# Optimization experiments

Measured on AMD Instinct MI355X. Metric: run time of the kernel, lower is better.

The kernel has to match this reference:

```python
import jax, jax.numpy as jnp
import numpy as np

B, T, D = 8, 1024, 768
H, HD = 12, 64
DFF = 3072
EPS = 1e-5


def setup_inputs() -> dict:
    key = jax.random.key(0)
    ks = jax.random.split(key, 6)
    s = lambda fan_in: 1.0 / np.sqrt(fan_in)
    return {
        "x": jax.random.normal(ks[0], (B, T, D), jnp.float32),
        "ln1_g": jnp.ones((D,), jnp.float32),
        "ln1_b": jnp.zeros((D,), jnp.float32),
        "w_qkv": jax.random.normal(ks[1], (D, 3 * D), jnp.float32) * s(D),
        "b_qkv": jnp.zeros((3 * D,), jnp.float32),
        "w_out": jax.random.normal(ks[2], (D, D), jnp.float32) * s(D),
        "b_out": jnp.zeros((D,), jnp.float32),
        "ln2_g": jnp.ones((D,), jnp.float32),
        "ln2_b": jnp.zeros((D,), jnp.float32),
        "w_fc1": jax.random.normal(ks[3], (D, DFF), jnp.float32) * s(D),
        "b_fc1": jnp.zeros((DFF,), jnp.float32),
        "w_fc2": jax.random.normal(ks[4], (DFF, D), jnp.float32) * s(DFF),
        "b_fc2": jnp.zeros((D,), jnp.float32),
    }


def _layernorm(x, g, b):
    mu = jnp.mean(x, axis=-1, keepdims=True)
    var = jnp.var(x, axis=-1, keepdims=True)
    return (x - mu) * jax.lax.rsqrt(var + EPS) * g + b


def reference(x, ln1_g, ln1_b, w_qkv, b_qkv, w_out, b_out,
              ln2_g, ln2_b, w_fc1, b_fc1, w_fc2, b_fc2):
    # --- attention branch (pre-norm) ---
    h = _layernorm(x, ln1_g, ln1_b)
    qkv = h @ w_qkv + b_qkv                      # [B,T,3D]
    q, k, v = jnp.split(qkv, 3, axis=-1)
    # [B,T,D] -> [B,H,T,HD]
    re = lambda t: t.reshape(B, T, H, HD).transpose(0, 2, 1, 3)
    q, k, v = re(q), re(k), re(v)
    scores = jnp.einsum("bhqd,bhkd->bhqk", q, k) * (1.0 / np.sqrt(HD))
    causal = jnp.tril(jnp.ones((T, T), bool))    # [T,T]
    scores = jnp.where(causal, scores, -jnp.inf)
    attn_weights = jax.nn.softmax(scores, axis=-1)  # [B,H,T,T]
    out = jnp.einsum("bhqk,bhkd->bhqd", attn_weights, v)
    out = out.transpose(0, 2, 1, 3).reshape(B, T, D)
    attn_out = out @ w_out + b_out
    x = x + attn_out
    # --- MLP branch (pre-norm) ---
    h2 = _layernorm(x, ln2_g, ln2_b)
    ff = jax.nn.gelu(h2 @ w_fc1 + b_fc1, approximate=False) @ w_fc2 + b_fc2
    x = x + ff
    return x, attn_weights
```

## Files before the change

kernel.cpp:

```cpp
#include <hip/hip_runtime.h>
#include <cstdint>
#include <cstddef>

namespace {

constexpr int Bb  = 8;
constexpr int Tt  = 1024;
constexpr int Dd  = 768;
constexpr int Hh  = 12;
constexpr int DFF = 3072;
constexpr int BT  = Bb * Tt;

typedef __attribute__((ext_vector_type(8))) short bf16x8;
typedef __attribute__((ext_vector_type(4))) short bf16x4;
typedef __attribute__((ext_vector_type(4))) float f32x4;

__device__ __forceinline__ short f2bf(float f) {
  union { float f; unsigned u; } v; v.f = f;
  unsigned r = v.u + 0x7fffu + ((v.u >> 16) & 1u);
  return (short)(r >> 16);
}
__device__ __forceinline__ float gelu_exact(float v) {
  return 0.5f * v * (1.0f + erff(v * 0.70710678118654752f));
}

#define MFMA16(a, b, c) __builtin_amdgcn_mfma_f32_16x16x32_bf16(a, b, c, 0, 0, 0)

__device__ __forceinline__ void gl_lds16(const short* g, short* l) {
  __builtin_amdgcn_global_load_lds(
      (const __attribute__((address_space(1))) unsigned int*)(g),
      (__attribute__((address_space(3))) unsigned int*)(l), 16, 0, 0);
}

__device__ __forceinline__ void cvt_body(float (*tile)[33],
                                         const float* __restrict__ in,
                                         short* __restrict__ out,
                                         int K, int N, int bx, int by) {
  int k0 = bx * 32, n0 = by * 32;
  int tx = threadIdx.x & 31, ty = threadIdx.x >> 5;
  #pragma unroll
  for (int r = ty; r < 32; r += 8)
    tile[r][tx] = in[(size_t)(k0 + r) * N + n0 + tx];
  __syncthreads();
  #pragma unroll
  for (int r = ty; r < 32; r += 8)
    out[(size_t)(n0 + r) * K + k0 + tx] = f2bf(tile[tx][r]);
}

__device__ __forceinline__ void ln_body(const float* __restrict__ x,
                                        const float* __restrict__ g,
                                        const float* __restrict__ b,
                                        short* __restrict__ out, int blkrow) {
  int lane = threadIdx.x & 63, wid = threadIdx.x >> 6;
  int row = blkrow * 4 + wid;
  const float* xr = x + (size_t)row * Dd;
  float v[12];
  float s = 0.f, ss = 0.f;
  #pragma unroll
  for (int c = 0; c < 3; c++) {
    float4 t = *(const float4*)&xr[c * 256 + lane * 4];
    v[c * 4 + 0] = t.x; v[c * 4 + 1] = t.y; v[c * 4 + 2] = t.z; v[c * 4 + 3] = t.w;
    s  += t.x + t.y + t.z + t.w;
    ss += t.x * t.x + t.y * t.y + t.z * t.z + t.w * t.w;
  }
  #pragma unroll
  for (int off = 1; off < 64; off <<= 1) {
    s += __shfl_xor(s, off); ss += __shfl_xor(ss, off);
  }
  float mu   = s * (1.f / Dd);
  float var  = ss * (1.f / Dd) - mu * mu;
  float rstd = rsqrtf(var + 1e-5f);
  #pragma unroll
  for (int c = 0; c < 3; c++) {
    bf16x4 o;
    #pragma unroll
    for (int j = 0; j < 4; j++) {
      int d = c * 256 + lane * 4 + j;
      o[j] = f2bf((v[c * 4 + j] - mu) * rstd * g[d] + b[d]);
    }
    *(bf16x4*)&out[(size_t)row * Dd + c * 256 + lane * 4] = o;
  }
}

__global__ __launch_bounds__(256) void prep(const float* __restrict__ w_qkv, short* wqkvT,
                                            const float* __restrict__ w_out, short* woutT,
                                            const float* __restrict__ w_fc1, short* wfc1T,
                                            const float* __restrict__ w_fc2, short* wfc2T,
                                            const float* __restrict__ x,
                                            const float* __restrict__ g,
                                            const float* __restrict__ b,
                                            short* __restrict__ h) {
  __shared__ float tile[32][33];
  int j = blockIdx.x;
  if (j < 1728)      cvt_body(tile, w_qkv, wqkvT, 768, 2304, j % 24, j / 24);
  else if (j < 2304) { int t = j - 1728; cvt_body(tile, w_out, woutT, 768, 768, t % 24, t / 24); }
  else if (j < 4608) { int t = j - 2304; cvt_body(tile, w_fc1, wfc1T, 768, 3072, t % 24, t / 24); }
  else if (j < 6912) { int t = j - 4608; cvt_body(tile, w_fc2, wfc2T, 3072, 768, t % 96, t / 96); }
  else               ln_body(x, g, b, h, j - 6912);
}

__global__ __launch_bounds__(256) void ln_rows(const float* __restrict__ x,
                                               const float* __restrict__ g,
                                               const float* __restrict__ b,
                                               short* __restrict__ out) {
  ln_body(x, g, b, out, blockIdx.x);
}

template <int EPI, int N, bool VTR>
__global__ __launch_bounds__(256) void gemm_bt(const short* __restrict__ A,
                                               const short* __restrict__ Bt,
                                               const float* __restrict__ bias,
                                               const float* __restrict__ add,
                                               void* __restrict__ outp,
                                               int K,
                                               short* __restrict__ vt) {
  __shared__ short S[17408];
  short* As0 = S;
  short* As1 = S + 4096;
  short* Bs0 = S + 8192;
  short* Bs1 = S + 12288;

  int nbx = gridDim.x;
  int flat = blockIdx.y * nbx + blockIdx.x;
  int cpx = (nbx * gridDim.y) >> 3;
  int swz = (flat & 7) * cpx + (flat >> 3);
  int m0 = (swz % nbx) * 128, n0 = (swz / nbx) * 128;

  int tid = threadIdx.x;
  int lane = tid & 63, wid = tid >> 6;
  int wm = wid >> 1, wn = wid & 1;
  int l15 = lane & 15, lg = lane >> 4;

  int jr = tid >> 2, jc = (tid & 3) << 3;
  int ldsb = wid << 9;

  auto stage = [&](short* Ad, short* Bd, int k0) {
    gl_lds16(&A[(size_t)(m0 + jr) * K + k0 + jc],       Ad + ldsb);
    gl_lds16(&A[(size_t)(m0 + 64 + jr) * K + k0 + jc],  Ad + 2048 + ldsb);
    gl_lds16(&Bt[(size_t)(n0 + jr) * K + k0 + jc],      Bd + ldsb);
    gl_lds16(&Bt[(size_t)(n0 + 64 + jr) * K + k0 + jc], Bd + 2048 + ldsb);
  };

  f32x4 acc[4][4] = {};
  stage(As0, Bs0, 0);
  int nk = K >> 5;
  for (int t = 0; t < nk; ++t) {
    short* Ab = (t & 1) ? As1 : As0;
    short* Bb = (t & 1) ? Bs1 : Bs0;
    if (t + 1 < nk) {
      stage((t & 1) ? As0 : As1, (t & 1) ? Bs0 : Bs1, (t + 1) << 5);
      asm volatile("s_waitcnt vmcnt(4)" ::: "memory");
    } else {
      asm volatile("s_waitcnt vmcnt(0)" ::: "memory");
    }
    __syncthreads();
    bf16x8 af[4], bfr[4];
    #pragma unroll
    for (int i = 0; i < 4; i++) af[i]  = *(bf16x8*)&Ab[(wm * 64 + i * 16 + l15) * 32 + lg * 8];
    #pragma unroll
    for (int j = 0; j < 4; j++) bfr[j] = *(bf16x8*)&Bb[(wn * 64 + j * 16 + l15) * 32 + lg * 8];
    #pragma unroll
    for (int i = 0; i < 4; i++)
      #pragma unroll
      for (int j = 0; j < 4; j++)
        acc[i][j] = MFMA16(af[i], bfr[j], acc[i][j]);
    __syncthreads();
  }

  if (EPI == 0 || EPI == 2) {
    short (*Cl)[136] = (short (*)[136])S;
    #pragma unroll
    for (int i = 0; i < 4; i++)
      #pragma unroll
      for (int j = 0; j < 4; j++)
        #pragma unroll
        for (int r = 0; r < 4; r++) {
          int row = wm * 64 + i * 16 + lg * 4 + r;
          int col = wn * 64 + j * 16 + l15;
          float vv = acc[i][j][r] + bias[n0 + col];
          if (EPI == 2) vv = gelu_exact(vv);
          int ch = col >> 3, co = col & 7;
          Cl[row][((ch ^ (row & 7)) << 3) | co] = f2bf(vv);
        }
    __syncthreads();
    if (VTR && n0 >= 1536) {
      int b = m0 >> 10, tbase = m0 & 1023;
      int h0 = (n0 - 1536) >> 6;
      #pragma unroll
      for (int half = 0; half < 2; ++half) {
        int c = (tid >> 2) + half * 64;
        int hh = c >> 6, d = c & 63;
        short* dst = vt + ((size_t)((b * Hh + h0 + hh) * 64 + d)) * Tt
                        + tbase + (tid & 3) * 32;
        #pragma unroll
        for (int j = 0; j < 4; ++j) {
          bf16x8 v8;
          #pragma unroll
          for (int k = 0; k < 8; ++k) {
            int t = (tid & 3) * 32 + j * 8 + k;
            v8[k] = Cl[t][(((c >> 3) ^ (t & 7)) << 3) | (c & 7)];
          }
          *(bf16x8*)(dst + j * 8) = v8;
        }
      }
    } else {
      int row = tid >> 1;
      int cb = (tid & 1) * 8;
      #pragma unroll
      for (int c = 0; c < 8; c++) {
        int ch = cb + c;
        bf16x8 v8 = *(bf16x8*)&Cl[row][(ch ^ (row & 7)) << 3];
        *(bf16x8*)&((short*)outp)[(size_t)(m0 + row) * N + n0 + (ch << 3)] = v8;
      }
    }
  } else {
    #pragma unroll
    for (int i = 0; i < 4; i++)
      #pragma unroll
      for (int j = 0; j < 4; j++)
        #pragma unroll
        for (int r = 0; r < 4; r++) {
          int m = m0 + wm * 64 + i * 16 + lg * 4 + r;
          int n = n0 + wn * 64 + j * 16 + l15;
          float vv = acc[i][j][r] + bias[n];
          size_t idx = (size_t)m * N + n;
          float ov = vv + add[idx];
          if (EPI == 3) __builtin_nontemporal_store(ov, &((float*)outp)[idx]);
          else          ((float*)outp)[idx] = ov;
        }
  }
}

template <int EPI>
__global__ __launch_bounds__(256) void gemm_n64(const short* __restrict__ A,
                                                const short* __restrict__ Bt,
                                                const float* __restrict__ bias,
                                                const float* __restrict__ add,
                                                float* __restrict__ outp,
                                                int K) {
  constexpr int N = 768;
  __shared__ short S[12288];
  short* As0 = S;
  short* As1 = S + 2048;
  short* Bs0 = S + 4096;
  short* Bs1 = S + 8192;

  int nbx = gridDim.x;
  int flat = blockIdx.y * nbx + blockIdx.x;
  int cpx = (nbx * gridDim.y) >> 3;
  int swz = (flat & 7) * cpx + (flat >> 3);
  int m0 = (swz % nbx) * 64, n0 = (swz / nbx) * 128;

  int tid = threadIdx.x;
  int lane = tid & 63, wid = tid >> 6;
  int wm = wid & 1, wn = wid >> 1;
  int l15 = lane & 15, lg = lane >> 4;

  int jr = tid >> 2, jc = (tid & 3) << 3;
  int ldsb = wid << 9;

  auto stage = [&](short* Ad, short* Bd, int k0) {
    gl_lds16(&A[(size_t)(m0 + jr) * K + k0 + jc],       Ad + ldsb);
    gl_lds16(&Bt[(size_t)(n0 + jr) * K + k0 + jc],      Bd + ldsb);
    gl_lds16(&Bt[(size_t)(n0 + 64 + jr) * K + k0 + jc], Bd + 2048 + ldsb);
  };

  f32x4 acc[2][4] = {};
  stage(As0, Bs0, 0);
  int nk = K >> 5;
  for (int t = 0; t < nk; ++t) {
    short* Ab = (t & 1) ? As1 : As0;
    short* Bb = (t & 1) ? Bs1 : Bs0;
    if (t + 1 < nk) {
      stage((t & 1) ? As0 : As1, (t & 1) ? Bs0 : Bs1, (t + 1) << 5);
      asm volatile("s_waitcnt vmcnt(3)" ::: "memory");
    } else {
      asm volatile("s_waitcnt vmcnt(0)" ::: "memory");
    }
    __syncthreads();
    bf16x8 af[2], bfr[4];
    #pragma unroll
    for (int i = 0; i < 2; i++) af[i]  = *(bf16x8*)&Ab[(wm * 32 + i * 16 + l15) * 32 + lg * 8];
    #pragma unroll
    for (int j = 0; j < 4; j++) bfr[j] = *(bf16x8*)&Bb[(wn * 64 + j * 16 + l15) * 32 + lg * 8];
    #pragma unroll
    for (int i = 0; i < 2; i++)
      #pragma unroll
      for (int j = 0; j < 4; j++)
        acc[i][j] = MFMA16(af[i], bfr[j], acc[i][j]);
    __syncthreads();
  }

  #pragma unroll
  for (int i = 0; i < 2; i++)
    #pragma unroll
    for (int j = 0; j < 4; j++)
      #pragma unroll
      for (int r = 0; r < 4; r++) {
        int m = m0 + wm * 32 + i * 16 + lg * 4 + r;
        int n = n0 + wn * 64 + j * 16 + l15;
        float vv = acc[i][j][r] + bias[n];
        size_t idx = (size_t)m * N + n;
        float ov = vv + add[idx];
        if (EPI == 3) __builtin_nontemporal_store(ov, &outp[idx]);
        else          outp[idx] = ov;
      }
}

template <int EPI>
__global__ __launch_bounds__(256) void gemm_n64k64(const short* __restrict__ A,
                                                   const short* __restrict__ Bt,
                                                   const float* __restrict__ bias,
                                                   const float* __restrict__ add,
                                                   float* __restrict__ outp,
                                                   int K) {
  constexpr int N = 768;
  __shared__ short S[24576];
  short* As0 = S;
  short* As1 = S + 4096;
  short* Bs0 = S + 8192;
  short* Bs1 = S + 16384;

  int nbx = gridDim.x;
  int flat = blockIdx.y * nbx + blockIdx.x;
  int cpx = (nbx * gridDim.y) >> 3;
  int swz = (flat & 7) * cpx + (flat >> 3);
  int m0 = (swz % nbx) * 64, n0 = (swz / nbx) * 128;

  int tid = threadIdx.x;
  int lane = tid & 63, wid = tid >> 6;
  int wm = wid & 1, wn = wid >> 1;
  int l15 = lane & 15, lg = lane >> 4;

  int r8 = tid >> 3;
  int gsl = (tid & 7) ^ (r8 & 7);
  int wb = wid << 9;

  auto stage = [&](short* Ad, short* Bd, int k0) {
    #pragma unroll
    for (int c = 0; c < 2; ++c)
      gl_lds16(&A[(size_t)(m0 + c * 32 + r8) * K + k0 + gsl * 8], Ad + c * 2048 + wb);
    #pragma unroll
    for (int c = 0; c < 4; ++c)
      gl_lds16(&Bt[(size_t)(n0 + c * 32 + r8) * K + k0 + gsl * 8], Bd + c * 2048 + wb);
  };

  f32x4 acc[2][4] = {};
  stage(As0, Bs0, 0);
  int nk = K >> 6;
  for (int t = 0; t < nk; ++t) {
    short* Ab = (t & 1) ? As1 : As0;
    short* Bb = (t & 1) ? Bs1 : Bs0;
    if (t + 1 < nk) {
      stage((t & 1) ? As0 : As1, (t & 1) ? Bs0 : Bs1, (t + 1) << 6);
      asm volatile("s_waitcnt vmcnt(6)" ::: "memory");
    } else {
      asm volatile("s_waitcnt vmcnt(0)" ::: "memory");
    }
    __syncthreads();
    bf16x8 af[2][2], bfr[4][2];
    #pragma unroll
    for (int i = 0; i < 2; i++) {
      int r = wm * 32 + i * 16 + l15;
      #pragma unroll
      for (int kk = 0; kk < 2; kk++)
        af[i][kk] = *(bf16x8*)&Ab[r * 64 + (((kk * 4 + lg) ^ (r & 7)) << 3)];
    }
    #pragma unroll
    for (int j = 0; j < 4; j++) {
      int r = wn * 64 + j * 16 + l15;
      #pragma unroll
      for (int kk = 0; kk < 2; kk++)
        bfr[j][kk] = *(bf16x8*)&Bb[r * 64 + (((kk * 4 + lg) ^ (r & 7)) << 3)];
    }
    #pragma unroll
    for (int kk = 0; kk < 2; kk++)
      #pragma unroll
      for (int i = 0; i < 2; i++)
        #pragma unroll
        for (int j = 0; j < 4; j++)
          acc[i][j] = MFMA16(af[i][kk], bfr[j][kk], acc[i][j]);
    __syncthreads();
  }

  #pragma unroll
  for (int i = 0; i < 2; i++)
    #pragma unroll
    for (int j = 0; j < 4; j++)
      #pragma unroll
      for (int r = 0; r < 4; r++) {
        int m = m0 + wm * 32 + i * 16 + lg * 4 + r;
        int n = n0 + wn * 64 + j * 16 + l15;
        float vv = acc[i][j][r] + bias[n];
        size_t idx = (size_t)m * N + n;
        float ov = vv + add[idx];
        if (EPI == 3) __builtin_nontemporal_store(ov, &outp[idx]);
        else          outp[idx] = ov;
      }
}

__global__ __launch_bounds__(256) void attn_fused(const short* __restrict__ qkv,
                                                  const short* __restrict__ vt,
                                                  float* __restrict__ attw,
                                                  short* __restrict__ ctx) {
  __shared__ short VtL[2][4096];
  __shared__ float Pf[4][16][68];
  int flat = blockIdx.y * 16 + blockIdx.x;
  int xcd = flat & 7, rr0 = flat >> 3;
  int bh   = xcd * 12 + (rr0 >> 4);
  int tile = 15 - (rr0 & 15);
  int q0 = tile * 64;
  int b = bh / Hh, h = bh % Hh;
  int tid = threadIdx.x, lane = tid & 63, wid = tid >> 6;
  int l15 = lane & 15, lg = lane >> 4;
  const short* base = qkv + (size_t)b * Tt * 2304;

  bf16x8 qa[2];
  {
    const short* qp = base + (size_t)(q0 + wid * 16 + l15) * 2304 + h * 64 + lg * 8;
    qa[0] = *(const bf16x8*)qp;
    qa[1] = *(const bf16x8*)(qp + 32);
  }

  float l[4] = {0.f, 0.f, 0.f, 0.f};
  for (int kt = 0; kt <= tile; ++kt) {
    f32x4 acc[4] = {};
    #pragma unroll
    for (int nf = 0; nf < 4; ++nf) {
      const short* kp = base + (size_t)(kt * 64 + nf * 16 + l15) * 2304 + 768 + h * 64 + lg * 8;
      bf16x8 k0 = *(const bf16x8*)kp;
      bf16x8 k1 = *(const bf16x8*)(kp + 32);
      acc[nf] = MFMA16(qa[0], k0, acc[nf]);
      acc[nf] = MFMA16(qa[1], k1, acc[nf]);
    }
    #pragma unroll
    for (int r = 0; r < 4; r++) {
      int qg = q0 + wid * 16 + lg * 4 + r;
      #pragma unroll
      for (int nf = 0; nf < 4; nf++) {
        int kg = kt * 64 + nf * 16 + l15;
        l[r] += (kg <= qg) ? __expf(acc[nf][r] * 0.125f) : 0.f;
      }
    }
  }
  float rl[4];
  #pragma unroll
  for (int r = 0; r < 4; r++) {
    float s = l[r];
    #pragma unroll
    for (int off = 1; off < 16; off <<= 1) s += __shfl_xor(s, off);
    rl[r] = 1.f / s;
  }

  const short* vtb = vt + (size_t)bh * 64 * Tt;
  int dS = wid * 16 + (lane >> 3);
  int cS = (lane & 7) ^ (lane >> 3);
  auto stageV = [&](int bi, int kt) {
    gl_lds16(&vtb[(size_t)dS * Tt + kt * 64 + cS * 8],       &VtL[bi][wid * 1024]);
    gl_lds16(&vtb[(size_t)(dS + 8) * Tt + kt * 64 + cS * 8], &VtL[bi][wid * 1024 + 512]);
  };

  f32x4 oacc[4] = {};
  stageV(0, 0);
  for (int kt = 0; kt <= tile; ++kt) {
    int cur = kt & 1;
    f32x4 acc[4] = {};
    #pragma unroll
    for (int nf = 0; nf < 4; nf++) {
      const short* kp = base + (size_t)(kt * 64 + nf * 16 + l15) * 2304 + 768 + h * 64 + lg * 8;
      bf16x8 k0 = *(const bf16x8*)kp;
      bf16x8 k1 = *(const bf16x8*)(kp + 32);
      acc[nf] = MFMA16(qa[0], k0, acc[nf]);
      acc[nf] = MFMA16(qa[1], k1, acc[nf]);
    }
    #pragma unroll
    for (int nf = 0; nf < 4; nf++) {
      #pragma unroll
      for (int r = 0; r < 4; r++) {
        int qg = q0 + wid * 16 + lg * 4 + r;
        int kg = kt * 64 + nf * 16 + l15;
        float p = (kg <= qg) ? __expf(acc[nf][r] * 0.125f) * rl[r] : 0.f;
        Pf[wid][lg * 4 + r][nf * 16 + l15] = p;
      }
    }
    asm volatile("s_waitcnt lgkmcnt(0)" ::: "memory");
    __builtin_amdgcn_sched_barrier(0);
    #pragma unroll
    for (int it = 0; it < 4; ++it) {
      int pr = it * 4 + lg;
      f32x4 pv = *(f32x4*)&Pf[wid][pr][l15 * 4];
      __builtin_nontemporal_store(
          pv, (f32x4*)&attw[((size_t)bh * Tt + q0 + wid * 16 + pr) * Tt + kt * 64 + l15 * 4]);
    }
    f32x4 pf0 = *(f32x4*)&Pf[wid][l15][lg * 8];
    f32x4 pf1 = *(f32x4*)&Pf[wid][l15][lg * 8 + 4];
    f32x4 pf2 = *(f32x4*)&Pf[wid][l15][lg * 8 + 32];
    f32x4 pf3 = *(f32x4*)&Pf[wid][l15][lg * 8 + 36];
    bf16x8 pa0, pa1;
    #pragma unroll
    for (int j = 0; j < 4; j++) {
      pa0[j] = f2bf(pf0[j]); pa0[4 + j] = f2bf(pf1[j]);
      pa1[j] = f2bf(pf2[j]); pa1[4 + j] = f2bf(pf3[j]);
    }
    asm volatile("s_waitcnt vmcnt(4)" ::: "memory");
    __builtin_amdgcn_s_barrier();
    __builtin_amdgcn_sched_barrier(0);
    if (kt < tile) stageV(cur ^ 1, kt + 1);
    #pragma unroll
    for (int nf = 0; nf < 4; nf++) {
      int dA = nf * 16 + l15;
      int sw = dA & 7;
      bf16x8 vb0 = *(bf16x8*)&VtL[cur][dA * 64 + ((lg ^ sw) << 3)];
      bf16x8 vb1 = *(bf16x8*)&VtL[cur][dA * 64 + (((4 + lg) ^ sw) << 3)];
      oacc[nf] = MFMA16(pa0, vb0, oacc[nf]);
      oacc[nf] = MFMA16(pa1, vb1, oacc[nf]);
    }
  }
  f32x4 z = {0.f, 0.f, 0.f, 0.f};
  for (int kt = tile + 1; kt < 16; ++kt) {
    #pragma unroll
    for (int it = 0; it < 4; ++it) {
      int pr = it * 4 + lg;
      __builtin_nontemporal_store(
          z, (f32x4*)&attw[((size_t)bh * Tt + q0 + wid * 16 + pr) * Tt + kt * 64 + l15 * 4]);
    }
  }
  #pragma unroll
  for (int nf = 0; nf < 4; nf++) {
    #pragma unroll
    for (int r = 0; r < 4; r++) {
      int t = q0 + wid * 16 + lg * 4 + r;
      ctx[((size_t)b * Tt + t) * Dd + h * 64 + nf * 16 + l15] = f2bf(oacc[nf][r]);
    }
  }
}

}

extern "C" void kernel_launch(void* const* d_in, const int* in_sizes, int n_in,
                              void* d_out, int out_size, void* d_ws, size_t ws_size,
                              hipStream_t stream) {
  const float* x     = (const float*)d_in[0];
  const float* ln1g  = (const float*)d_in[1];
  const float* ln1b  = (const float*)d_in[2];
  const float* w_qkv = (const float*)d_in[3];
  const float* b_qkv = (const float*)d_in[4];
  const float* w_out = (const float*)d_in[5];
  const float* b_out = (const float*)d_in[6];
  const float* ln2g  = (const float*)d_in[7];
  const float* ln2b  = (const float*)d_in[8];
  const float* w_fc1 = (const float*)d_in[9];
  const float* b_fc1 = (const float*)d_in[10];
  const float* w_fc2 = (const float*)d_in[11];
  const float* b_fc2 = (const float*)d_in[12];

  char* ws = (char*)d_ws;
  size_t o = 0;
  short* wqkvT = (short*)(ws + o); o += (size_t)2304 * 768 * 2;
  short* woutT = (short*)(ws + o); o += (size_t)768 * 768 * 2;
  short* wfc1T = (short*)(ws + o); o += (size_t)3072 * 768 * 2;
  short* wfc2T = (short*)(ws + o); o += (size_t)768 * 3072 * 2;
  short* h     = (short*)(ws + o); o += (size_t)BT * Dd * 2;
  short* qkv   = (short*)(ws + o); o += (size_t)BT * 2304 * 2;
  float* y1    = (float*)(ws + o); o += (size_t)BT * Dd * 4;
  short* h2    = (short*)(ws + o); o += (size_t)BT * Dd * 2;
  short* vt    = (short*)(ws + o); o += (size_t)96 * 64 * Tt * 2;
  short* ctx  = h;
  short* gbuf = h;

  float* out_x = (float*)d_out;
  float* attw  = out_x + (size_t)BT * Dd;

  prep<<<8960, 256, 0, stream>>>(w_qkv, wqkvT, w_out, woutT, w_fc1, wfc1T,
                                 w_fc2, wfc2T, x, ln1g, ln1b, h);
  gemm_bt<0, 2304, true><<<dim3(BT / 128, 2304 / 128), 256, 0, stream>>>(
      h, wqkvT, b_qkv, nullptr, qkv, 768, vt);
  attn_fused<<<dim3(16, 96), 256, 0, stream>>>(qkv, vt, attw, ctx);
  gemm_n64<1><<<dim3(BT / 64, 768 / 128), 256, 0, stream>>>(ctx, woutT, b_out, x, y1, 768);
  ln_rows<<<BT / 4, 256, 0, stream>>>(y1, ln2g, ln2b, h2);
  gemm_bt<2, 3072, false><<<dim3(BT / 128, 3072 / 128), 256, 0, stream>>>(
      h2, wfc1T, b_fc1, nullptr, gbuf, 768, nullptr);
  gemm_n64k64<3><<<dim3(BT / 64, 768 / 128), 256, 0, stream>>>(gbuf, wfc2T, b_fc2, y1, out_x, 3072);
}
```

Baseline: 405.9 us.

## Run FC1 with the 64-row K64 GEMM and store attention probabilities in bf16 LDS

FC1 now uses the gemm_n64k64 kernel, with N as a template parameter and a new GELU epilogue. That epilogue converts to bf16, stages the tile through swizzled LDS and writes 16-byte coalesced stores. This replaces the 128x128 gemm_bt path and gives FC1 more blocks and a different tile shape. In attention, the probability tile is kept in LDS as bf16 instead of fp32, which halves the LDS traffic and lets the MFMA operands be read directly without conversion. The attention weights written to global memory are now bf16-rounded values widened back to fp32, so output precision drops slightly.

```diff
diff --git a/kernel.cpp b/kernel.cpp
--- a/kernel.cpp
+++ b/kernel.cpp
@@ -19,6 +19,11 @@
   union { float f; unsigned u; } v; v.f = f;
   unsigned r = v.u + 0x7fffu + ((v.u >> 16) & 1u);
   return (short)(r >> 16);
+}
+__device__ __forceinline__ float bf2f(short s) {
+  union { unsigned u; float f; } v;
+  v.u = ((unsigned)(unsigned short)s) << 16;
+  return v.f;
 }
 __device__ __forceinline__ float gelu_exact(float v) {
   return 0.5f * v * (1.0f + erff(v * 0.70710678118654752f));
@@ -307,14 +312,13 @@
       }
 }
 
-template <int EPI>
+template <int EPI, int N>
 __global__ __launch_bounds__(256) void gemm_n64k64(const short* __restrict__ A,
                                                    const short* __restrict__ Bt,
                                                    const float* __restrict__ bias,
                                                    const float* __restrict__ add,
-                                                   float* __restrict__ outp,
+                                                   void* __restrict__ outp,
                                                    int K) {
-  constexpr int N = 768;
   __shared__ short S[24576];
   short* As0 = S;
   short* As1 = S + 4096;
@@ -383,20 +387,43 @@
     __syncthreads();
   }
 
-  #pragma unroll
-  for (int i = 0; i < 2; i++)
-    #pragma unroll
-    for (int j = 0; j < 4; j++)
-      #pragma unroll
-      for (int r = 0; r < 4; r++) {
-        int m = m0 + wm * 32 + i * 16 + lg * 4 + r;
-        int n = n0 + wn * 64 + j * 16 + l15;
-        float vv = acc[i][j][r] + bias[n];
-        size_t idx = (size_t)m * N + n;
-        float ov = vv + add[idx];
-        if (EPI == 3) __builtin_nontemporal_store(ov, &outp[idx]);
-        else          outp[idx] = ov;
-      }
+  if (EPI == 2) {
+    short (*Cl)[136] = (short (*)[136])S;
+    #pragma unroll
+    for (int i = 0; i < 2; i++)
+      #pragma unroll
+      for (int j = 0; j < 4; j++)
+        #pragma unroll
+        for (int r = 0; r < 4; r++) {
+          int row = wm * 32 + i * 16 + lg * 4 + r;
+          int col = wn * 64 + j * 16 + l15;
+          float vv = gelu_exact(acc[i][j][r] + bias[n0 + col]);
+          int ch = col >> 3, co = col & 7;
+          Cl[row][((ch ^ (row & 7)) << 3) | co] = f2bf(vv);
+        }
+    __syncthreads();
+    int row = tid >> 2;
+    #pragma unroll
+    for (int c = 0; c < 4; c++) {
+      int ch = (tid & 3) + c * 4;
+      bf16x8 v8 = *(bf16x8*)&Cl[row][(ch ^ (row & 7)) << 3];
+      *(bf16x8*)&((short*)outp)[(size_t)(m0 + row) * N + n0 + (ch << 3)] = v8;
+    }
+  } else {
+    #pragma unroll
+    for (int i = 0; i < 2; i++)
+      #pragma unroll
+      for (int j = 0; j < 4; j++)
+        #pragma unroll
+        for (int r = 0; r < 4; r++) {
+          int m = m0 + wm * 32 + i * 16 + lg * 4 + r;
+          int n = n0 + wn * 64 + j * 16 + l15;
+          float vv = acc[i][j][r] + bias[n];
+          size_t idx = (size_t)m * N + n;
+          float ov = vv + add[idx];
+          __builtin_nontemporal_store(ov, &((float*)outp)[idx]);
+        }
+  }
 }
 
 __global__ __launch_bounds__(256) void attn_fused(const short* __restrict__ qkv,
@@ -404,7 +431,7 @@
                                                   float* __restrict__ attw,
                                                   short* __restrict__ ctx) {
   __shared__ short VtL[2][4096];
-  __shared__ float Pf[4][16][68];
+  __shared__ short Pb[4][16][72];
   int flat = blockIdx.y * 16 + blockIdx.x;
   int xcd = flat & 7, rr0 = flat >> 3;
   int bh   = xcd * 12 + (rr0 >> 4);
@@ -480,28 +507,25 @@
         int qg = q0 + wid * 16 + lg * 4 + r;
         int kg = kt * 64 + nf * 16 + l15;
         float p = (kg <= qg) ? __expf(acc[nf][r] * 0.125f) * rl[r] : 0.f;
-        Pf[wid][lg * 4 + r][nf * 16 + l15] = p;
+        Pb[wid][lg * 4 + r][nf * 16 + l15] = f2bf(p);
       }
     }
     asm volatile("s_waitcnt lgkmcnt(0)" ::: "memory");
     __builtin_amdgcn_sched_barrier(0);
     #pragma unroll
-    for (int it = 0; it < 4; ++it) {
-      int pr = it * 4 + lg;
-      f32x4 pv = *(f32x4*)&Pf[wid][pr][l15 * 4];
-      __builtin_nontemporal_store(
-          pv, (f32x4*)&attw[((size_t)bh * Tt + q0 + wid * 16 + pr) * Tt + kt * 64 + l15 * 4]);
-    }
-    f32x4 pf0 = *(f32x4*)&Pf[wid][l15][lg * 8];
-    f32x4 pf1 = *(f32x4*)&Pf[wid][l15][lg * 8 + 4];
-    f32x4 pf2 = *(f32x4*)&Pf[wid][l15][lg * 8 + 32];
-    f32x4 pf3 = *(f32x4*)&Pf[wid][l15][lg * 8 + 36];
-    bf16x8 pa0, pa1;
-    #pragma unroll
-    for (int j = 0; j < 4; j++) {
-      pa0[j] = f2bf(pf0[j]); pa0[4 + j] = f2bf(pf1[j]);
-      pa1[j] = f2bf(pf2[j]); pa1[4 + j] = f2bf(pf3[j]);
-    }
+    for (int it = 0; it < 2; ++it) {
+      int pr = it * 8 + (lane >> 3);
+      int cb = (lane & 7) * 8;
+      bf16x8 pv = *(bf16x8*)&Pb[wid][pr][cb];
+      f32x4 lo, hi;
+      #pragma unroll
+      for (int j = 0; j < 4; j++) { lo[j] = bf2f(pv[j]); hi[j] = bf2f(pv[4 + j]); }
+      float* dst = &attw[((size_t)bh * Tt + q0 + wid * 16 + pr) * Tt + kt * 64 + cb];
+      __builtin_nontemporal_store(lo, (f32x4*)dst);
+      __builtin_nontemporal_store(hi, (f32x4*)(dst + 4));
+    }
+    bf16x8 pa0 = *(bf16x8*)&Pb[wid][l15][lg * 8];
+    bf16x8 pa1 = *(bf16x8*)&Pb[wid][l15][lg * 8 + 32];
     asm volatile("s_waitcnt vmcnt(4)" ::: "memory");
     __builtin_amdgcn_s_barrier();
     __builtin_amdgcn_sched_barrier(0);
@@ -578,7 +602,8 @@
   attn_fused<<<dim3(16, 96), 256, 0, stream>>>(qkv, vt, attw, ctx);
   gemm_n64<1><<<dim3(BT / 64, 768 / 128), 256, 0, stream>>>(ctx, woutT, b_out, x, y1, 768);
   ln_rows<<<BT / 4, 256, 0, stream>>>(y1, ln2g, ln2b, h2);
-  gemm_bt<2, 3072, false><<<dim3(BT / 128, 3072 / 128), 256, 0, stream>>>(
-      h2, wfc1T, b_fc1, nullptr, gbuf, 768, nullptr);
-  gemm_n64k64<3><<<dim3(BT / 64, 768 / 128), 256, 0, stream>>>(gbuf, wfc2T, b_fc2, y1, out_x, 3072);
-}
+  gemm_n64k64<2, DFF><<<dim3(BT / 64, DFF / 128), 256, 0, stream>>>(
+      h2, wfc1T, b_fc1, nullptr, gbuf, 768);
+  gemm_n64k64<3, 768><<<dim3(BT / 64, 768 / 128), 256, 0, stream>>>(
+      gbuf, wfc2T, b_fc2, y1, out_x, 3072);
+}
```

After: 413.3 us. About the same (+1.8%).
